# Optimization experiments

Measured on AMD Instinct MI355X. Metric: run time of the kernel, lower is better.

Reference implementation:

```python
import jax, jax.numpy as jnp
import numpy as np

N, E = 50000, 800000
DIN, DH, DOUT = 128, 128, 64


def setup_inputs() -> dict:
    key = jax.random.key(0)
    k = jax.random.split(key, 6)
    node_features = jax.random.normal(k[0], (N, DIN), dtype=jnp.float32)
    edge_src = jax.random.randint(k[1], (E,), 0, N)
    edge_dst = jax.random.randint(k[2], (E,), 0, N)
    # Glorot-ish init for the two GCNConv weight matrices, zero bias (PyG default bias=True)
    W1 = jax.random.normal(k[3], (DIN, DH), dtype=jnp.float32) * (1.0 / np.sqrt(DIN))
    b1 = jnp.zeros((DH,), dtype=jnp.float32)
    W2 = jax.random.normal(k[4], (DH, DOUT), dtype=jnp.float32) * (1.0 / np.sqrt(DH))
    b2 = jnp.zeros((DOUT,), dtype=jnp.float32)
    return {"node_features": node_features, "edge_src": edge_src, "edge_dst": edge_dst,
            "W1": W1, "b1": b1, "W2": W2, "b2": b2}


def gcn_conv(x, W, b, src, dst, n):
    """PyG GCNConv: add self-loops, symmetric D^-1/2 (A+I) D^-1/2 normalization."""
    xw = x @ W  # [n, d_out]
    loops = jnp.arange(n, dtype=src.dtype)
    s = jnp.concatenate([src, loops])  # edges + self-loops
    d = jnp.concatenate([dst, loops])
    deg = jax.ops.segment_sum(jnp.ones_like(d, dtype=xw.dtype), d, num_segments=n)
    dinv = jnp.where(deg > 0, jax.lax.rsqrt(deg), 0.0)
    norm = dinv[s] * dinv[d]  # [E + n]
    msg = xw[s] * norm[:, None]  # gather + scale (memory-bound)
    out = jax.ops.segment_sum(msg, d, num_segments=n)  # scatter-add
    return out + b


def reference(node_features, edge_src, edge_dst, W1, b1, W2, b2):
    n = node_features.shape[0]
    h = gcn_conv(node_features, W1, b1, edge_src, edge_dst, n)
    h = jax.nn.relu(h)  # dropout omitted (inference / eval mode)
    h = gcn_conv(h, W2, b2, edge_src, edge_dst, n)
    # EdgePredictor: per-edge dot product of endpoint representations
    score = jnp.sum(h[edge_src] * h[edge_dst], axis=-1)  # [E]
    return score
```

## Files before the change

kernel.cpp:

```cpp
#include <hip/hip_runtime.h>
#include <hip/hip_bf16.h>
#include <type_traits>


#define DIN 128
#define DH  128
#define DOUT 64
#define BSH 7
#define BNODES 128
#define CAP 2560
#define QSH 13
#define POISON 0xAAAAAAAAu

typedef __attribute__((ext_vector_type(8))) short short8;
typedef __attribute__((ext_vector_type(4))) float floatx4;

__device__ inline float2 bf2_to_f2(unsigned u) {
    union { unsigned i; float f; } a, b;
    a.i = u << 16;
    b.i = u & 0xffff0000u;
    return make_float2(a.f, b.f);
}
__device__ inline float bf_to_f(unsigned short u) {
    union { unsigned i; float f; } a;
    a.i = ((unsigned)u) << 16;
    return a.f;
}
__device__ inline unsigned short f_to_bf(float f) {
    union { float f; unsigned i; } v; v.f = f;
    unsigned r = v.i + 0x7fffu + ((v.i >> 16) & 1u);
    return (unsigned short)(r >> 16);
}

__global__ __launch_bounds__(256) void place_gemm1_kernel(
    const int* __restrict__ src, const int* __restrict__ dst,
    unsigned* __restrict__ cursor, uint2* __restrict__ tmp, int E, int EB,
    const float* __restrict__ X, const float* __restrict__ W1,
    unsigned short* __restrict__ Y, int nrows) {
    __shared__ __align__(16) char smem[69632];
    int bid = blockIdx.x, t = threadIdx.x;

    if (bid < EB) {
        int* hist = (int*)smem;
        int* cur  = hist + 512;
        hist[t] = 0; hist[t + 256] = 0;
        __syncthreads();
        int base = bid * 4096 + t;
        int d[16];
#pragma unroll
        for (int it = 0; it < 16; ++it) {
            int e = base + it * 256;
            d[it] = (e < E) ? dst[e] : -1;
            if (d[it] >= 0) atomicAdd(&hist[d[it] >> BSH], 1);
        }
        __syncthreads();
#pragma unroll
        for (int k = t; k < 512; k += 256)
            if (hist[k])
                cur[k] = (int)(atomicAdd(&cursor[k], (unsigned)hist[k]) - POISON);
        __syncthreads();
#pragma unroll
        for (int it = 0; it < 16; ++it) {
            int e = base + it * 256;
            if (d[it] >= 0) {
                int bkt = d[it] >> BSH;
                int r = atomicAdd(&cur[bkt], 1);
                if (r >= 0 && r < CAP)
                    tmp[(size_t)bkt * CAP + r] =
                        make_uint2((unsigned)src[e] |
                                   ((unsigned)(d[it] & (BNODES - 1)) << 16),
                                   (unsigned)e);
            }
        }
        return;
    }

    constexpr int KP = 136;
    unsigned short* Xs = (unsigned short*)smem;
    unsigned short* Wt = Xs + 128 * KP;
    int row0 = (bid - EB) * 128;

#pragma unroll
    for (int it = 0; it < 16; ++it) {
        int idx = it * 256 + t;
        int r = idx >> 5;
        int c4 = (idx & 31) * 4;
        int gr = row0 + r; if (gr >= nrows) gr = nrows - 1;
        float4 v = *(const float4*)(X + (size_t)gr * 128 + c4);
        ushort4 p;
        p.x = f_to_bf(v.x); p.y = f_to_bf(v.y);
        p.z = f_to_bf(v.z); p.w = f_to_bf(v.w);
        *(ushort4*)&Xs[r * KP + c4] = p;
    }
#pragma unroll
    for (int it = 0; it < 16; ++it) {
        int idx = it * 256 + t;
        int n = idx >> 5;
        int k4 = (idx & 31) * 4;
        ushort4 p;
        p.x = f_to_bf(W1[(size_t)(k4 + 0) * 128 + n]);
        p.y = f_to_bf(W1[(size_t)(k4 + 1) * 128 + n]);
        p.z = f_to_bf(W1[(size_t)(k4 + 2) * 128 + n]);
        p.w = f_to_bf(W1[(size_t)(k4 + 3) * 128 + n]);
        *(ushort4*)&Wt[n * KP + k4] = p;
    }
    __syncthreads();

    int wv = t >> 6, lane = t & 63;
    int lr = lane & 15;
    int lk = (lane >> 4) * 8;
    int rw = wv * 32;

    floatx4 acc[2][8];
#pragma unroll
    for (int rt = 0; rt < 2; ++rt)
#pragma unroll
        for (int ct = 0; ct < 8; ++ct) acc[rt][ct] = (floatx4){0.f, 0.f, 0.f, 0.f};

#pragma unroll
    for (int kk = 0; kk < 128; kk += 32) {
        short8 a[2], b[8];
#pragma unroll
        for (int rt = 0; rt < 2; ++rt)
            a[rt] = *(const short8*)&Xs[(rw + rt * 16 + lr) * KP + kk + lk];
#pragma unroll
        for (int ct = 0; ct < 8; ++ct)
            b[ct] = *(const short8*)&Wt[(ct * 16 + lr) * KP + kk + lk];
#pragma unroll
        for (int rt = 0; rt < 2; ++rt)
#pragma unroll
            for (int ct = 0; ct < 8; ++ct)
                acc[rt][ct] = __builtin_amdgcn_mfma_f32_16x16x32_bf16(
                    a[rt], b[ct], acc[rt][ct], 0, 0, 0);
    }
#pragma unroll
    for (int rt = 0; rt < 2; ++rt) {
#pragma unroll
        for (int i = 0; i < 4; ++i) {
            int grow = row0 + rw + rt * 16 + (lane >> 4) * 4 + i;
            if (grow >= nrows) continue;
#pragma unroll
            for (int ct = 0; ct < 8; ++ct)
                Y[(size_t)grow * 128 + ct * 16 + lr] = f_to_bf(acc[rt][ct][i]);
        }
    }
}

__global__ __launch_bounds__(512) void bucket_csr_kernel(const uint2* __restrict__ tmp,
                                                         const unsigned* __restrict__ cursor,
                                                         int* __restrict__ row_beg,
                                                         int* __restrict__ row_end,
                                                         float* __restrict__ dinv,
                                                         int* __restrict__ col,
                                                         int* __restrict__ eidx, int N) {
    __shared__ int hist[1024], cur[1024];
    __shared__ int wsum[8];
    __shared__ unsigned ebuf[CAP];
    __shared__ unsigned ibuf[CAP];
    __shared__ unsigned ssrc[CAP];
    __shared__ unsigned sidx[CAP];
    int b = blockIdx.x, t = threadIdx.x;
    int lane = t & 63, wv = t >> 6;
    int size = (int)(cursor[b] - POISON);
    if (size < 0) size = 0;
    if (size > CAP) size = CAP;
    size_t rbase = (size_t)b * CAP;
    hist[t] = 0; hist[t + 512] = 0;
    __syncthreads();
    for (int i = t; i < size; i += 512) {
        uint2 e = tmp[rbase + i];
        ebuf[i] = e.x;
        ibuf[i] = e.y;
        int key = (int)(e.x >> 16) * 8 + (int)((e.x & 0xffffu) >> QSH);
        atomicAdd(&hist[key], 1);
    }
    __syncthreads();
    int l0 = hist[t * 2], l1 = hist[t * 2 + 1];
    int s = l0 + l1;
    int run = s;
#pragma unroll
    for (int off = 1; off < 64; off <<= 1) {
        int u = __shfl_up(run, off);
        if (lane >= off) run += u;
    }
    if (lane == 63) wsum[wv] = run;
    __syncthreads();
    int woff = 0;
#pragma unroll
    for (int k = 0; k < 8; ++k) woff += (k < wv) ? wsum[k] : 0;
    int excl = woff + run - s;
    hist[t * 2] = excl;       cur[t * 2] = excl;
    hist[t * 2 + 1] = excl + l0; cur[t * 2 + 1] = excl + l0;
    __syncthreads();
    if (t < BNODES) {
        int node = b * BNODES + t;
        if (node < N) {
            int nbeg = hist[t * 8];
            int nend = (t == BNODES - 1) ? size : hist[t * 8 + 8];
            row_beg[node] = (int)rbase + nbeg;
            row_end[node] = (int)rbase + nend;
            dinv[node] = rsqrtf((float)(nend - nbeg + 1));
        }
    }
    __syncthreads();
    for (int i = t; i < size; i += 512) {
        unsigned e = ebuf[i];
        int key = (int)(e >> 16) * 8 + (int)((e & 0xffffu) >> QSH);
        int r = atomicAdd(&cur[key], 1);
        ssrc[r] = e & 0xffffu;
        sidx[r] = ibuf[i];
    }
    __syncthreads();
    for (int i = t; i < size; i += 512) {
        col[rbase + i]  = (int)ssrc[i];
        eidx[rbase + i] = (int)sidx[i];
    }
}

__global__ __launch_bounds__(256, 8) void agg1_kernel(const unsigned short* __restrict__ y1,
                                                      const int* __restrict__ row_beg,
                                                      const int* __restrict__ row_end,
                                                      const int* __restrict__ col,
                                                      const float* __restrict__ dinv,
                                                      const float* __restrict__ b1,
                                                      unsigned short* __restrict__ h1, int n) {
    int w = (blockIdx.x * 256 + threadIdx.x) >> 6;
    int lane = threadIdx.x & 63;
    if (w >= n) return;
    int q = lane & 15;
    int g = lane >> 4;
    float dw = dinv[w];
    float acc[8];
    {
        uint4 hv = *(const uint4*)(y1 + (size_t)w * 128 + q * 8);
        float selfw = (g == 0) ? dw : 0.f;
        float2 f;
        f = bf2_to_f2(hv.x); acc[0] = selfw * f.x; acc[1] = selfw * f.y;
        f = bf2_to_f2(hv.y); acc[2] = selfw * f.x; acc[3] = selfw * f.y;
        f = bf2_to_f2(hv.z); acc[4] = selfw * f.x; acc[5] = selfw * f.y;
        f = bf2_to_f2(hv.w); acc[6] = selfw * f.x; acc[7] = selfw * f.y;
    }
    int beg = row_beg[w], end = row_end[w];
    int i = beg;
    for (; i + 16 <= end; i += 16) {
        int s4[4];
#pragma unroll
        for (int u = 0; u < 4; ++u) s4[u] = col[i + u * 4 + g];
        float dv[4];
#pragma unroll
        for (int u = 0; u < 4; ++u) dv[u] = dinv[s4[u]];
        uint4 tv[4];
#pragma unroll
        for (int u = 0; u < 4; ++u)
            tv[u] = *(const uint4*)(y1 + (size_t)s4[u] * 128 + q * 8);
#pragma unroll
        for (int u = 0; u < 4; ++u) {
            float2 f;
            f = bf2_to_f2(tv[u].x); acc[0] = fmaf(dv[u], f.x, acc[0]); acc[1] = fmaf(dv[u], f.y, acc[1]);
            f = bf2_to_f2(tv[u].y); acc[2] = fmaf(dv[u], f.x, acc[2]); acc[3] = fmaf(dv[u], f.y, acc[3]);
            f = bf2_to_f2(tv[u].z); acc[4] = fmaf(dv[u], f.x, acc[4]); acc[5] = fmaf(dv[u], f.y, acc[5]);
            f = bf2_to_f2(tv[u].w); acc[6] = fmaf(dv[u], f.x, acc[6]); acc[7] = fmaf(dv[u], f.y, acc[7]);
        }
    }
    for (; i < end; i += 4) {
        int r = i + g;
        bool ok = r < end;
        int sv = ok ? col[r] : col[i];
        float dv = ok ? dinv[sv] : 0.f;
        uint4 tv = *(const uint4*)(y1 + (size_t)sv * 128 + q * 8);
        float2 f;
        f = bf2_to_f2(tv.x); acc[0] = fmaf(dv, f.x, acc[0]); acc[1] = fmaf(dv, f.y, acc[1]);
        f = bf2_to_f2(tv.y); acc[2] = fmaf(dv, f.x, acc[2]); acc[3] = fmaf(dv, f.y, acc[3]);
        f = bf2_to_f2(tv.z); acc[4] = fmaf(dv, f.x, acc[4]); acc[5] = fmaf(dv, f.y, acc[5]);
        f = bf2_to_f2(tv.w); acc[6] = fmaf(dv, f.x, acc[6]); acc[7] = fmaf(dv, f.y, acc[7]);
    }
#pragma unroll
    for (int j = 0; j < 8; ++j) {
        acc[j] += __shfl_xor(acc[j], 16);
        acc[j] += __shfl_xor(acc[j], 32);
    }
    if (g == 0) {
        float r0 = fmaxf(fmaf(dw, acc[0], b1[q * 8 + 0]), 0.f);
        float r1 = fmaxf(fmaf(dw, acc[1], b1[q * 8 + 1]), 0.f);
        float r2 = fmaxf(fmaf(dw, acc[2], b1[q * 8 + 2]), 0.f);
        float r3 = fmaxf(fmaf(dw, acc[3], b1[q * 8 + 3]), 0.f);
        float r4 = fmaxf(fmaf(dw, acc[4], b1[q * 8 + 4]), 0.f);
        float r5 = fmaxf(fmaf(dw, acc[5], b1[q * 8 + 5]), 0.f);
        float r6 = fmaxf(fmaf(dw, acc[6], b1[q * 8 + 6]), 0.f);
        float r7 = fmaxf(fmaf(dw, acc[7], b1[q * 8 + 7]), 0.f);
        uint4 pk;
        pk.x = (unsigned)f_to_bf(r0) | ((unsigned)f_to_bf(r1) << 16);
        pk.y = (unsigned)f_to_bf(r2) | ((unsigned)f_to_bf(r3) << 16);
        pk.z = (unsigned)f_to_bf(r4) | ((unsigned)f_to_bf(r5) << 16);
        pk.w = (unsigned)f_to_bf(r6) | ((unsigned)f_to_bf(r7) << 16);
        *(uint4*)(h1 + (size_t)w * 128 + q * 8) = pk;
    }
}

__global__ __launch_bounds__(256) void mfma_gemm2_kernel(const unsigned short* __restrict__ X,
                                                         const float* __restrict__ W,
                                                         const float* __restrict__ dinv,
                                                         unsigned short* __restrict__ Y,
                                                         int nrows) {
    constexpr int KP = 136;
    __shared__ unsigned short Xs[128 * KP];
    __shared__ unsigned short Wt[64 * KP];
    int tid = threadIdx.x;
    int row0 = blockIdx.x * 128;

#pragma unroll
    for (int it = 0; it < 8; ++it) {
        int idx = it * 256 + tid;
        int r = idx >> 4;
        int c8 = (idx & 15) * 8;
        int gr = row0 + r; if (gr >= nrows) gr = nrows - 1;
        uint4 v = *(const uint4*)(X + (size_t)gr * 128 + c8);
        *(uint4*)&Xs[r * KP + c8] = v;
    }
#pragma unroll
    for (int it = 0; it < 8; ++it) {
        int idx = it * 256 + tid;
        int n = idx >> 5;
        int k4 = (idx & 31) * 4;
        ushort4 p;
        p.x = f_to_bf(W[(size_t)(k4 + 0) * 64 + n]);
        p.y = f_to_bf(W[(size_t)(k4 + 1) * 64 + n]);
        p.z = f_to_bf(W[(size_t)(k4 + 2) * 64 + n]);
        p.w = f_to_bf(W[(size_t)(k4 + 3) * 64 + n]);
        *(ushort4*)&Wt[n * KP + k4] = p;
    }
    __syncthreads();

    int wv = tid >> 6, lane = tid & 63;
    int lr = lane & 15;
    int lk = (lane >> 4) * 8;
    int rw = wv * 32;

    floatx4 acc[2][4];
#pragma unroll
    for (int rt = 0; rt < 2; ++rt)
#pragma unroll
        for (int ct = 0; ct < 4; ++ct) acc[rt][ct] = (floatx4){0.f, 0.f, 0.f, 0.f};

#pragma unroll
    for (int kk = 0; kk < 128; kk += 32) {
        short8 a[2], b[4];
#pragma unroll
        for (int rt = 0; rt < 2; ++rt)
            a[rt] = *(const short8*)&Xs[(rw + rt * 16 + lr) * KP + kk + lk];
#pragma unroll
        for (int ct = 0; ct < 4; ++ct)
            b[ct] = *(const short8*)&Wt[(ct * 16 + lr) * KP + kk + lk];
#pragma unroll
        for (int rt = 0; rt < 2; ++rt)
#pragma unroll
            for (int ct = 0; ct < 4; ++ct)
                acc[rt][ct] = __builtin_amdgcn_mfma_f32_16x16x32_bf16(
                    a[rt], b[ct], acc[rt][ct], 0, 0, 0);
    }
#pragma unroll
    for (int rt = 0; rt < 2; ++rt) {
#pragma unroll
        for (int i = 0; i < 4; ++i) {
            int grow = row0 + rw + rt * 16 + (lane >> 4) * 4 + i;
            if (grow >= nrows) continue;
            float dv = dinv[grow];
#pragma unroll
            for (int ct = 0; ct < 4; ++ct)
                Y[(size_t)grow * 64 + ct * 16 + lr] = f_to_bf(acc[rt][ct][i] * dv);
        }
    }
}

__global__ __launch_bounds__(256, 8) void agg2_kernel(const unsigned short* __restrict__ y,
                                                      const int* __restrict__ row_beg,
                                                      const int* __restrict__ row_end,
                                                      const int* __restrict__ col,
                                                      const float* __restrict__ dinv,
                                                      const float* __restrict__ bias,
                                                      unsigned short* __restrict__ out, int n) {
    int w = (blockIdx.x * 256 + threadIdx.x) >> 6;
    int lane = threadIdx.x & 63;
    if (w >= n) return;
    int q = lane & 15;
    int g = lane >> 4;
    float acc[4];
    {
        uint2 sv = *(const uint2*)(y + (size_t)w * 64 + q * 4);
        float selfw = (g == 0) ? 1.f : 0.f;
        float2 f;
        f = bf2_to_f2(sv.x); acc[0] = selfw * f.x; acc[1] = selfw * f.y;
        f = bf2_to_f2(sv.y); acc[2] = selfw * f.x; acc[3] = selfw * f.y;
    }
    int beg = row_beg[w], end = row_end[w];
    int i = beg;
    for (; i + 32 <= end; i += 32) {
        int s8[8];
#pragma unroll
        for (int u = 0; u < 8; ++u) s8[u] = col[i + u * 4 + g];
        uint2 tv[8];
#pragma unroll
        for (int u = 0; u < 8; ++u)
            tv[u] = *(const uint2*)(y + (size_t)s8[u] * 64 + q * 4);
#pragma unroll
        for (int u = 0; u < 8; ++u) {
            float2 f;
            f = bf2_to_f2(tv[u].x); acc[0] += f.x; acc[1] += f.y;
            f = bf2_to_f2(tv[u].y); acc[2] += f.x; acc[3] += f.y;
        }
    }
    for (; i < end; i += 4) {
        int r = i + g;
        bool ok = r < end;
        int sv = ok ? col[r] : col[i];
        float m = ok ? 1.f : 0.f;
        uint2 tv = *(const uint2*)(y + (size_t)sv * 64 + q * 4);
        float2 f;
        f = bf2_to_f2(tv.x); acc[0] = fmaf(m, f.x, acc[0]); acc[1] = fmaf(m, f.y, acc[1]);
        f = bf2_to_f2(tv.y); acc[2] = fmaf(m, f.x, acc[2]); acc[3] = fmaf(m, f.y, acc[3]);
    }
#pragma unroll
    for (int j = 0; j < 4; ++j) {
        acc[j] += __shfl_xor(acc[j], 16);
        acc[j] += __shfl_xor(acc[j], 32);
    }
    if (g == 0) {
        float dw = dinv[w];
        float r0 = fmaf(dw, acc[0], bias[q * 4 + 0]);
        float r1 = fmaf(dw, acc[1], bias[q * 4 + 1]);
        float r2 = fmaf(dw, acc[2], bias[q * 4 + 2]);
        float r3 = fmaf(dw, acc[3], bias[q * 4 + 3]);
        uint2 pk;
        pk.x = (unsigned)f_to_bf(r0) | ((unsigned)f_to_bf(r1) << 16);
        pk.y = (unsigned)f_to_bf(r2) | ((unsigned)f_to_bf(r3) << 16);
        *(uint2*)(out + (size_t)w * 64 + q * 4) = pk;
    }
}

__global__ __launch_bounds__(256, 8) void score_csr_kernel(const unsigned short* __restrict__ h2,
                                                           const int* __restrict__ row_beg,
                                                           const int* __restrict__ row_end,
                                                           const int* __restrict__ col,
                                                           const int* __restrict__ eidx,
                                                           float* __restrict__ out, int n) {
    int w = (blockIdx.x * 256 + threadIdx.x) >> 6;
    int lane = threadIdx.x & 63;
    if (w >= n) return;
    int q = lane & 7;
    uint4 hd = *(const uint4*)(h2 + (size_t)w * 64 + q * 8);
    float d0[8];
    { float2 f;
      f = bf2_to_f2(hd.x); d0[0] = f.x; d0[1] = f.y;
      f = bf2_to_f2(hd.y); d0[2] = f.x; d0[3] = f.y;
      f = bf2_to_f2(hd.z); d0[4] = f.x; d0[5] = f.y;
      f = bf2_to_f2(hd.w); d0[6] = f.x; d0[7] = f.y; }
    int beg = row_beg[w], end = row_end[w];
    int g = lane >> 3;
    for (int i = beg; i < end; i += 16) {
        int ei0 = i + g, ei1 = i + 8 + g;
        bool ok0 = ei0 < end, ok1 = ei1 < end;
        int s0 = ok0 ? col[ei0] : col[i];
        int s1 = ok1 ? col[ei1] : col[i];
        uint4 hs0 = *(const uint4*)(h2 + (size_t)s0 * 64 + q * 8);
        uint4 hs1 = *(const uint4*)(h2 + (size_t)s1 * 64 + q * 8);
        float v0 = 0.f, v1 = 0.f;
        float2 f;
        f = bf2_to_f2(hs0.x); v0 = fmaf(d0[0], f.x, v0); v0 = fmaf(d0[1], f.y, v0);
        f = bf2_to_f2(hs0.y); v0 = fmaf(d0[2], f.x, v0); v0 = fmaf(d0[3], f.y, v0);
        f = bf2_to_f2(hs0.z); v0 = fmaf(d0[4], f.x, v0); v0 = fmaf(d0[5], f.y, v0);
        f = bf2_to_f2(hs0.w); v0 = fmaf(d0[6], f.x, v0); v0 = fmaf(d0[7], f.y, v0);
        f = bf2_to_f2(hs1.x); v1 = fmaf(d0[0], f.x, v1); v1 = fmaf(d0[1], f.y, v1);
        f = bf2_to_f2(hs1.y); v1 = fmaf(d0[2], f.x, v1); v1 = fmaf(d0[3], f.y, v1);
        f = bf2_to_f2(hs1.z); v1 = fmaf(d0[4], f.x, v1); v1 = fmaf(d0[5], f.y, v1);
        f = bf2_to_f2(hs1.w); v1 = fmaf(d0[6], f.x, v1); v1 = fmaf(d0[7], f.y, v1);
        v0 += __shfl_xor(v0, 4);
        v0 += __shfl_xor(v0, 2);
        v0 += __shfl_xor(v0, 1);
        v1 += __shfl_xor(v1, 4);
        v1 += __shfl_xor(v1, 2);
        v1 += __shfl_xor(v1, 1);
        if (ok0 && q == 0) out[eidx[ei0]] = v0;
        if (ok1 && q == 0) out[eidx[ei1]] = v1;
    }
}

extern "C" void kernel_launch(void* const* d_in, const int* in_sizes, int n_in,
                              void* d_out, int out_size, void* d_ws, size_t ws_size,
                              hipStream_t stream) {
    const float* X   = (const float*)d_in[0];
    const int*   src = (const int*)d_in[1];
    const int*   dst = (const int*)d_in[2];
    const float* W1  = (const float*)d_in[3];
    const float* b1  = (const float*)d_in[4];
    const float* W2  = (const float*)d_in[5];
    const float* b2  = (const float*)d_in[6];
    float* score = (float*)d_out;

    const int N = in_sizes[0] / DIN;
    const int E = in_sizes[1];
    const int nbuck = (N + BNODES - 1) / BNODES;
    const int EB = (E + 4095) / 4096;
    const int GB = (N + 127) / 128;

    auto align = [](size_t x) { return (x + 255) & ~(size_t)255; };
    char* p = (char*)d_ws;
    unsigned* cursor = (unsigned*)p;        p += align(512 * 4);
    int*   row_beg = (int*)p;               p += align((size_t)N * 4);
    int*   row_end = (int*)p;               p += align((size_t)N * 4);
    float* dinv    = (float*)p;             p += align((size_t)N * 4);
    int*   col     = (int*)p;               p += align((size_t)nbuck * CAP * 4);
    int*   eidx    = (int*)p;               p += align((size_t)nbuck * CAP * 4);
    uint2* tmp     = (uint2*)p;             p += align((size_t)nbuck * CAP * 8);
    unsigned short* y1 = (unsigned short*)p; p += align((size_t)N * DH * 2);
    unsigned short* h1 = (unsigned short*)p; p += align((size_t)N * DH * 2);
    unsigned short* y2 = y1;
    unsigned short* h2 = y1 + (size_t)N * DOUT;

    place_gemm1_kernel<<<EB + GB, 256, 0, stream>>>(src, dst, cursor, tmp, E, EB,
                                                    X, W1, y1, N);
    bucket_csr_kernel<<<nbuck, 512, 0, stream>>>(tmp, cursor, row_beg, row_end,
                                                 dinv, col, eidx, N);

    int agg_blocks = (N + 3) / 4;
    agg1_kernel<<<agg_blocks, 256, 0, stream>>>(y1, row_beg, row_end, col,
                                                dinv, b1, h1, N);

    mfma_gemm2_kernel<<<GB, 256, 0, stream>>>(h1, W2, dinv, y2, N);

    agg2_kernel<<<agg_blocks, 256, 0, stream>>>(y2, row_beg, row_end, col,
                                                dinv, b2, h2, N);
    score_csr_kernel<<<agg_blocks, 256, 0, stream>>>(h2, row_beg, row_end,
                                                     col, eidx, score, N);
}
```

Before: 222.5 us.

## Split GEMM1 tiles across placement and bucket-CSR kernels to balance load

The first-layer GEMM tiles are factored into a shared device helper and split in half. One half runs alongside edge placement and the other half runs as extra blocks in the bucket-CSR kernel. The bucket kernel drops from 512 to 256 threads with a shared-memory scan, so its blocks can co-run with the 256-thread GEMM blocks. The aim is to fill idle compute units during the small bucket kernel, at the cost of a slower LDS-barrier scan and fewer threads per bucket.

```diff
diff --git a/kernel.cpp b/kernel.cpp
--- a/kernel.cpp
+++ b/kernel.cpp
@@ -32,7 +32,81 @@
     return (unsigned short)(r >> 16);
 }
 
-__global__ __launch_bounds__(256) void place_gemm1_kernel(
+__device__ inline void gemm1_tile(char* smem, const float* __restrict__ X,
+                                  const float* __restrict__ W1,
+                                  unsigned short* __restrict__ Y,
+                                  int nrows, int row0, int t) {
+    constexpr int KP = 136;
+    unsigned short* Xs = (unsigned short*)smem;
+    unsigned short* Wt = Xs + 128 * KP;
+
+#pragma unroll
+    for (int it = 0; it < 16; ++it) {
+        int idx = it * 256 + t;
+        int r = idx >> 5;
+        int c4 = (idx & 31) * 4;
+        int gr = row0 + r; if (gr >= nrows) gr = nrows - 1;
+        float4 v = *(const float4*)(X + (size_t)gr * 128 + c4);
+        ushort4 p;
+        p.x = f_to_bf(v.x); p.y = f_to_bf(v.y);
+        p.z = f_to_bf(v.z); p.w = f_to_bf(v.w);
+        *(ushort4*)&Xs[r * KP + c4] = p;
+    }
+#pragma unroll
+    for (int it = 0; it < 16; ++it) {
+        int idx = it * 256 + t;
+        int n = idx >> 5;
+        int k4 = (idx & 31) * 4;
+        ushort4 p;
+        p.x = f_to_bf(W1[(size_t)(k4 + 0) * 128 + n]);
+        p.y = f_to_bf(W1[(size_t)(k4 + 1) * 128 + n]);
+        p.z = f_to_bf(W1[(size_t)(k4 + 2) * 128 + n]);
+        p.w = f_to_bf(W1[(size_t)(k4 + 3) * 128 + n]);
+        *(ushort4*)&Wt[n * KP + k4] = p;
+    }
+    __syncthreads();
+
+    int wv = t >> 6, lane = t & 63;
+    int lr = lane & 15;
+    int lk = (lane >> 4) * 8;
+    int rw = wv * 32;
+
+    floatx4 acc[2][8];
+#pragma unroll
+    for (int rt = 0; rt < 2; ++rt)
+#pragma unroll
+        for (int ct = 0; ct < 8; ++ct) acc[rt][ct] = (floatx4){0.f, 0.f, 0.f, 0.f};
+
+#pragma unroll
+    for (int kk = 0; kk < 128; kk += 32) {
+        short8 a[2], b[8];
+#pragma unroll
+        for (int rt = 0; rt < 2; ++rt)
+            a[rt] = *(const short8*)&Xs[(rw + rt * 16 + lr) * KP + kk + lk];
+#pragma unroll
+        for (int ct = 0; ct < 8; ++ct)
+            b[ct] = *(const short8*)&Wt[(ct * 16 + lr) * KP + kk + lk];
+#pragma unroll
+        for (int rt = 0; rt < 2; ++rt)
+#pragma unroll
+            for (int ct = 0; ct < 8; ++ct)
+                acc[rt][ct] = __builtin_amdgcn_mfma_f32_16x16x32_bf16(
+                    a[rt], b[ct], acc[rt][ct], 0, 0, 0);
+    }
+#pragma unroll
+    for (int rt = 0; rt < 2; ++rt) {
+#pragma unroll
+        for (int i = 0; i < 4; ++i) {
+            int grow = row0 + rw + rt * 16 + (lane >> 4) * 4 + i;
+            if (grow >= nrows) continue;
+#pragma unroll
+            for (int ct = 0; ct < 8; ++ct)
+                Y[(size_t)grow * 128 + ct * 16 + lr] = f_to_bf(acc[rt][ct][i]);
+        }
+    }
+}
+
+__global__ __launch_bounds__(256) void place_gemm1a_kernel(
     const int* __restrict__ src, const int* __restrict__ dst,
     unsigned* __restrict__ cursor, uint2* __restrict__ tmp, int E, int EB,
     const float* __restrict__ X, const float* __restrict__ W1,
@@ -74,100 +148,40 @@
         }
         return;
     }
-
-    constexpr int KP = 136;
-    unsigned short* Xs = (unsigned short*)smem;
-    unsigned short* Wt = Xs + 128 * KP;
-    int row0 = (bid - EB) * 128;
-
-#pragma unroll
-    for (int it = 0; it < 16; ++it) {
-        int idx = it * 256 + t;
-        int r = idx >> 5;
-        int c4 = (idx & 31) * 4;
-        int gr = row0 + r; if (gr >= nrows) gr = nrows - 1;
-        float4 v = *(const float4*)(X + (size_t)gr * 128 + c4);
-        ushort4 p;
-        p.x = f_to_bf(v.x); p.y = f_to_bf(v.y);
-        p.z = f_to_bf(v.z); p.w = f_to_bf(v.w);
-        *(ushort4*)&Xs[r * KP + c4] = p;
-    }
-#pragma unroll
-    for (int it = 0; it < 16; ++it) {
-        int idx = it * 256 + t;
-        int n = idx >> 5;
-        int k4 = (idx & 31) * 4;
-        ushort4 p;
-        p.x = f_to_bf(W1[(size_t)(k4 + 0) * 128 + n]);
-        p.y = f_to_bf(W1[(size_t)(k4 + 1) * 128 + n]);
-        p.z = f_to_bf(W1[(size_t)(k4 + 2) * 128 + n]);
-        p.w = f_to_bf(W1[(size_t)(k4 + 3) * 128 + n]);
-        *(ushort4*)&Wt[n * KP + k4] = p;
-    }
-    __syncthreads();
-
-    int wv = t >> 6, lane = t & 63;
-    int lr = lane & 15;
-    int lk = (lane >> 4) * 8;
-    int rw = wv * 32;
-
-    floatx4 acc[2][8];
-#pragma unroll
-    for (int rt = 0; rt < 2; ++rt)
-#pragma unroll
-        for (int ct = 0; ct < 8; ++ct) acc[rt][ct] = (floatx4){0.f, 0.f, 0.f, 0.f};
-
-#pragma unroll
-    for (int kk = 0; kk < 128; kk += 32) {
-        short8 a[2], b[8];
-#pragma unroll
-        for (int rt = 0; rt < 2; ++rt)
-            a[rt] = *(const short8*)&Xs[(rw + rt * 16 + lr) * KP + kk + lk];
-#pragma unroll
-        for (int ct = 0; ct < 8; ++ct)
-            b[ct] = *(const short8*)&Wt[(ct * 16 + lr) * KP + kk + lk];
-#pragma unroll
-        for (int rt = 0; rt < 2; ++rt)
-#pragma unroll
-            for (int ct = 0; ct < 8; ++ct)
-                acc[rt][ct] = __builtin_amdgcn_mfma_f32_16x16x32_bf16(
-                    a[rt], b[ct], acc[rt][ct], 0, 0, 0);
-    }
-#pragma unroll
-    for (int rt = 0; rt < 2; ++rt) {
-#pragma unroll
-        for (int i = 0; i < 4; ++i) {
-            int grow = row0 + rw + rt * 16 + (lane >> 4) * 4 + i;
-            if (grow >= nrows) continue;
-#pragma unroll
-            for (int ct = 0; ct < 8; ++ct)
-                Y[(size_t)grow * 128 + ct * 16 + lr] = f_to_bf(acc[rt][ct][i]);
-        }
-    }
-}
-
-__global__ __launch_bounds__(512) void bucket_csr_kernel(const uint2* __restrict__ tmp,
-                                                         const unsigned* __restrict__ cursor,
-                                                         int* __restrict__ row_beg,
-                                                         int* __restrict__ row_end,
-                                                         float* __restrict__ dinv,
-                                                         int* __restrict__ col,
-                                                         int* __restrict__ eidx, int N) {
-    __shared__ int hist[1024], cur[1024];
-    __shared__ int wsum[8];
-    __shared__ unsigned ebuf[CAP];
-    __shared__ unsigned ibuf[CAP];
-    __shared__ unsigned ssrc[CAP];
-    __shared__ unsigned sidx[CAP];
-    int b = blockIdx.x, t = threadIdx.x;
-    int lane = t & 63, wv = t >> 6;
+    gemm1_tile(smem, X, W1, Y, nrows, (bid - EB) * 128, t);
+}
+
+__global__ __launch_bounds__(256) void bucket_gemm1b_kernel(
+    const uint2* __restrict__ tmp, const unsigned* __restrict__ cursor,
+    int* __restrict__ row_beg, int* __restrict__ row_end,
+    float* __restrict__ dinv, int* __restrict__ col, int* __restrict__ eidx,
+    int N, int NB, int G1,
+    const float* __restrict__ X, const float* __restrict__ W1,
+    unsigned short* __restrict__ Y, int nrows) {
+    __shared__ __align__(16) char smem[69632];
+    int bid = blockIdx.x, t = threadIdx.x;
+
+    if (bid >= NB) {
+        gemm1_tile(smem, X, W1, Y, nrows, (G1 + bid - NB) * 128, t);
+        return;
+    }
+
+    int* hist = (int*)smem;
+    int* cur  = hist + 1024;
+    int* tsum = cur + 1024;
+    unsigned* ebuf = (unsigned*)(tsum + 256);
+    unsigned* ibuf = ebuf + CAP;
+    unsigned* ssrc = ibuf + CAP;
+    unsigned* sidx = ssrc + CAP;
+    int b = bid;
     int size = (int)(cursor[b] - POISON);
     if (size < 0) size = 0;
     if (size > CAP) size = CAP;
     size_t rbase = (size_t)b * CAP;
-    hist[t] = 0; hist[t + 512] = 0;
-    __syncthreads();
-    for (int i = t; i < size; i += 512) {
+#pragma unroll
+    for (int k = 0; k < 4; ++k) hist[t * 4 + k] = 0;
+    __syncthreads();
+    for (int i = t; i < size; i += 256) {
         uint2 e = tmp[rbase + i];
         ebuf[i] = e.x;
         ibuf[i] = e.y;
@@ -175,22 +189,25 @@
         atomicAdd(&hist[key], 1);
     }
     __syncthreads();
-    int l0 = hist[t * 2], l1 = hist[t * 2 + 1];
-    int s = l0 + l1;
-    int run = s;
-#pragma unroll
-    for (int off = 1; off < 64; off <<= 1) {
-        int u = __shfl_up(run, off);
-        if (lane >= off) run += u;
-    }
-    if (lane == 63) wsum[wv] = run;
-    __syncthreads();
-    int woff = 0;
-#pragma unroll
-    for (int k = 0; k < 8; ++k) woff += (k < wv) ? wsum[k] : 0;
-    int excl = woff + run - s;
-    hist[t * 2] = excl;       cur[t * 2] = excl;
-    hist[t * 2 + 1] = excl + l0; cur[t * 2 + 1] = excl + l0;
+    int local[4];
+    int s = 0;
+#pragma unroll
+    for (int k = 0; k < 4; ++k) { local[k] = hist[t * 4 + k]; s += local[k]; }
+    tsum[t] = s;
+    __syncthreads();
+    for (int off = 1; off < 256; off <<= 1) {
+        int u = (t >= off) ? tsum[t - off] : 0;
+        __syncthreads();
+        tsum[t] += u;
+        __syncthreads();
+    }
+    int run = tsum[t] - s;
+#pragma unroll
+    for (int k = 0; k < 4; ++k) {
+        hist[t * 4 + k] = run;
+        cur[t * 4 + k] = run;
+        run += local[k];
+    }
     __syncthreads();
     if (t < BNODES) {
         int node = b * BNODES + t;
@@ -203,7 +220,7 @@
         }
     }
     __syncthreads();
-    for (int i = t; i < size; i += 512) {
+    for (int i = t; i < size; i += 256) {
         unsigned e = ebuf[i];
         int key = (int)(e >> 16) * 8 + (int)((e & 0xffffu) >> QSH);
         int r = atomicAdd(&cur[key], 1);
@@ -211,7 +228,7 @@
         sidx[r] = ibuf[i];
     }
     __syncthreads();
-    for (int i = t; i < size; i += 512) {
+    for (int i = t; i < size; i += 256) {
         col[rbase + i]  = (int)ssrc[i];
         eidx[rbase + i] = (int)sidx[i];
     }
@@ -501,6 +518,8 @@
     const int nbuck = (N + BNODES - 1) / BNODES;
     const int EB = (E + 4095) / 4096;
     const int GB = (N + 127) / 128;
+    const int G1 = GB / 2;
+    const int G2 = GB - G1;
 
     auto align = [](size_t x) { return (x + 255) & ~(size_t)255; };
     char* p = (char*)d_ws;
@@ -516,10 +535,11 @@
     unsigned short* y2 = y1;
     unsigned short* h2 = y1 + (size_t)N * DOUT;
 
-    place_gemm1_kernel<<<EB + GB, 256, 0, stream>>>(src, dst, cursor, tmp, E, EB,
-                                                    X, W1, y1, N);
-    bucket_csr_kernel<<<nbuck, 512, 0, stream>>>(tmp, cursor, row_beg, row_end,
-                                                 dinv, col, eidx, N);
+    place_gemm1a_kernel<<<EB + G1, 256, 0, stream>>>(src, dst, cursor, tmp, E, EB,
+                                                     X, W1, y1, N);
+    bucket_gemm1b_kernel<<<nbuck + G2, 256, 0, stream>>>(tmp, cursor, row_beg,
+                                                         row_end, dinv, col, eidx,
+                                                         N, nbuck, G1, X, W1, y1, N);
 
     int agg_blocks = (N + 3) / 4;
     agg1_kernel<<<agg_blocks, 256, 0, stream>>>(y1, row_beg, row_end, col,
```

Result: slower. 240.8 us (+8.3%).
